# Optimization experiments

Hardware: AMD Instinct MI355X
Metric: run time of the kernel (lower is better)

The kernel has to match this reference:

```python
import jax, jax.numpy as jnp
import numpy as np

N_NODES = 50000
N_EDGES = 800000
IN_DIM = 128
HID = 128
HEADS = 4
OUT_DIM = 32
NEG_SLOPE = 0.2  # DGL GATConv default


def _gat_params(key, in_dim, out_feat, heads):
    k1, k2, k3 = jax.random.split(key, 3)
    s = 1.0 / np.sqrt(in_dim)
    W = jax.random.normal(k1, (in_dim, heads * out_feat), jnp.float32) * s
    attn_l = jax.random.normal(k2, (heads, out_feat), jnp.float32) * 0.1
    attn_r = jax.random.normal(k3, (heads, out_feat), jnp.float32) * 0.1
    b = jnp.zeros((heads * out_feat,), jnp.float32)
    return W, attn_l, attn_r, b


def setup_inputs() -> dict:
    key = jax.random.key(0)
    ks = jax.random.split(key, 10)
    inp = {
        "x_am": jax.random.normal(ks[0], (N_NODES, IN_DIM), jnp.float32),
        "x_ph": jax.random.normal(ks[1], (N_NODES, IN_DIM), jnp.float32),
        "exist": jax.random.uniform(ks[2], (N_EDGES,), jnp.float32),
        "am_exist": jax.random.uniform(ks[3], (N_EDGES,), jnp.float32),
        "src": jax.random.randint(ks[4], (N_EDGES,), 0, N_NODES, jnp.int32),
        "dst": jax.random.randint(ks[5], (N_EDGES,), 0, N_NODES, jnp.int32),
    }
    # layer 0 (input_dim -> hidden//head per head), layer 1 (hidden -> output_dim per head)
    inp["W0a"], inp["al0a"], inp["ar0a"], inp["b0a"] = _gat_params(ks[6], IN_DIM, HID // HEADS, HEADS)
    inp["W0p"], inp["al0p"], inp["ar0p"], inp["b0p"] = _gat_params(ks[7], IN_DIM, HID // HEADS, HEADS)
    inp["W1a"], inp["al1a"], inp["ar1a"], inp["b1a"] = _gat_params(ks[8], HID, OUT_DIM, HEADS)
    inp["W1p"], inp["al1p"], inp["ar1p"], inp["b1p"] = _gat_params(ks[9], HID, OUT_DIM, HEADS)
    return inp


def gat_conv(x, src, dst, W, attn_l, attn_r, b, edge_w, n_nodes):
    """DGL-style GATConv with edge_weight: out[i] = sum_{e: dst=i} softmax_i(LeakyReLU(el[src]+er[dst])) * w_e * ft[src]."""
    heads, outf = attn_l.shape
    ft = (x @ W).reshape(-1, heads, outf)                 # (N, H, F)
    el = jnp.sum(ft * attn_l, axis=-1)                    # (N, H)
    er = jnp.sum(ft * attn_r, axis=-1)                    # (N, H)
    e = jax.nn.leaky_relu(el[src] + er[dst], NEG_SLOPE)   # (E, H)
    emax = jax.ops.segment_max(e, dst, num_segments=n_nodes)
    emax = jnp.where(jnp.isfinite(emax), emax, 0.0)       # guard isolated nodes
    ex = jnp.exp(e - emax[dst])
    denom = jax.ops.segment_sum(ex, dst, num_segments=n_nodes)
    a = ex / jnp.maximum(denom[dst], 1e-9)                # edge softmax over incoming edges
    a = a * edge_w[:, None]                               # post-softmax edge weighting
    out = jax.ops.segment_sum(ft[src] * a[:, :, None], dst, num_segments=n_nodes)  # (N, H, F)
    return out + b.reshape(heads, outf)


def reference(x_am, x_ph, exist, am_exist,
              W0a, al0a, ar0a, b0a, W0p, al0p, ar0p, b0p,
              W1a, al1a, ar1a, b1a, W1p, al1p, ar1p, b1p,
              src, dst):
    n = x_am.shape[0]
    # layer 0: GATConv -> flatten -> ReLU (dropout rate 0 in eval)
    h_am = gat_conv(x_am, src, dst, W0a, al0a, ar0a, b0a, am_exist, n)
    h_ph = gat_conv(x_ph, src, dst, W0p, al0p, ar0p, b0p, exist, n)
    h_am = jax.nn.relu(h_am.reshape(n, -1))
    h_ph = jax.nn.relu(h_ph.reshape(n, -1))
    # layer 1 (last): GATConv -> mean over heads
    h_am = gat_conv(h_am, src, dst, W1a, al1a, ar1a, b1a, am_exist, n).mean(axis=1)
    h_ph = gat_conv(h_ph, src, dst, W1p, al1p, ar1p, b1p, exist, n).mean(axis=1)
    return (h_am, h_ph)
```

## Files before the change

kernel.cpp:

```cpp
#include <hip/hip_runtime.h>
#include <hip/hip_fp16.h>


typedef _Float16 f16x8 __attribute__((ext_vector_type(8)));
typedef float f32x4 __attribute__((ext_vector_type(4)));

struct GemmP { const void* X; const __half* Wt; const float *al, *ar; __half* Y; float *el, *er; };
struct ChP   { const __half* ft; const float *el, *er, *bias; void* out; };

__global__ void init_kernel(int* __restrict__ zero, int nzero,
                            const float* __restrict__ W0a, const float* __restrict__ W0p,
                            const float* __restrict__ W1a, const float* __restrict__ W1p,
                            __half* __restrict__ Wt) {
  int i = blockIdx.x * 256 + threadIdx.x;
  if (i < nzero) zero[i] = 0;
  {
    int m = i >> 14, idx = i & 16383;
    const float* W = (m == 0) ? W0a : (m == 1) ? W0p : (m == 2) ? W1a : W1p;
    int nn = idx >> 7, k = idx & 127;
    Wt[(size_t)m * 16384 + nn * 128 + k] = __float2half_rn(W[k * 128 + nn]);
  }
}

__global__ __launch_bounds__(256) void scan_kernel(const int* __restrict__ counts,
                                                   int* __restrict__ offsets,
                                                   int* __restrict__ sync,
                                                   int nb_stride, int n, int E) {
  __shared__ int lds[256];
  __shared__ int sbid, sprev;
  int* state = sync + 64;
  int* agg = state + nb_stride;
  int* incl = agg + nb_stride;
  int t = threadIdx.x;
  if (t == 0) sbid = atomicAdd(sync, 1);
  __syncthreads();
  int bid = sbid;
  int i = bid * 256 + t;
  int v = (i < n) ? counts[i] : 0;
  lds[t] = v;
  __syncthreads();
  for (int off = 1; off < 256; off <<= 1) {
    int x = (t >= off) ? lds[t - off] : 0;
    __syncthreads();
    lds[t] += x;
    __syncthreads();
  }
  int total = lds[255];
  if (t == 0) {
    if (bid == 0) {
      __hip_atomic_store(&incl[0], total, __ATOMIC_RELAXED, __HIP_MEMORY_SCOPE_AGENT);
      __hip_atomic_store(&state[0], 2, __ATOMIC_RELEASE, __HIP_MEMORY_SCOPE_AGENT);
      sprev = 0;
    } else {
      __hip_atomic_store(&agg[bid], total, __ATOMIC_RELAXED, __HIP_MEMORY_SCOPE_AGENT);
      __hip_atomic_store(&state[bid], 1, __ATOMIC_RELEASE, __HIP_MEMORY_SCOPE_AGENT);
    }
  }
  if (bid > 0 && t < 64) {
    int run = 0;
    int base = bid - 1;
    while (true) {
      int idx = base - t;
      int st = 2, val = 0;
      if (idx >= 0) {
        do {
          st = __hip_atomic_load(&state[idx], __ATOMIC_ACQUIRE, __HIP_MEMORY_SCOPE_AGENT);
        } while (st == 0);
        val = (st == 2)
                  ? __hip_atomic_load(&incl[idx], __ATOMIC_RELAXED, __HIP_MEMORY_SCOPE_AGENT)
                  : __hip_atomic_load(&agg[idx], __ATOMIC_RELAXED, __HIP_MEMORY_SCOPE_AGENT);
      }
      unsigned long long done = __ballot(st == 2);
      int firstDone = (int)__ffsll(done) - 1;
      int contrib = (firstDone < 0) ? val : ((t <= firstDone) ? val : 0);
#pragma unroll
      for (int o = 1; o < 64; o <<= 1) contrib += __shfl_xor(contrib, o);
      run += contrib;
      if (firstDone >= 0) break;
      base -= 64;
    }
    if (t == 0) {
      __hip_atomic_store(&incl[bid], run + total, __ATOMIC_RELAXED, __HIP_MEMORY_SCOPE_AGENT);
      __hip_atomic_store(&state[bid], 2, __ATOMIC_RELEASE, __HIP_MEMORY_SCOPE_AGENT);
      sprev = run;
    }
  }
  __syncthreads();
  int prev = sprev;
  if (i < n) offsets[i] = prev + lds[t] - v;
  if (i == 0) offsets[n] = E;
}

__global__ void fill_kernel(const int* __restrict__ src, const int* __restrict__ dst,
                            const float* __restrict__ exist, const float* __restrict__ am_exist,
                            const int* __restrict__ offs, const int* __restrict__ rank,
                            int4* __restrict__ edge16, int E) {
  int e = blockIdx.x * blockDim.x + threadIdx.x;
  if (e >= E) return;
  int d = dst[e];
  int pos = offs[d] + rank[e];
  edge16[pos] = make_int4(src[e], d, __float_as_int(am_exist[e]), __float_as_int(exist[e]));
}

template <int AFP16>
__device__ __forceinline__ void gemm_body(GemmP p, int bx, int n) {
  constexpr int LDH = 72;
  constexpr int LDE = 136;
  __shared__ __half lds[2 * 128 * LDH];
  __half* As = lds;
  __half* Ws = lds + 128 * LDH;
  int t = threadIdx.x;
  int row0 = bx << 7;
  int wv = t >> 6, lane = t & 63;
  int m = lane & 15, q = lane >> 4;

  f32x4 acc[2][8];
#pragma unroll
  for (int rt = 0; rt < 2; ++rt)
#pragma unroll
    for (int ct = 0; ct < 8; ++ct) acc[rt][ct] = (f32x4){0.f, 0.f, 0.f, 0.f};

#pragma unroll
  for (int kh = 0; kh < 2; ++kh) {
    __syncthreads();
    if (AFP16) {
      const __half* Xh = (const __half*)p.X;
#pragma unroll
      for (int i = 0; i < 4; ++i) {
        int c = t + (i << 8);
        int r = c >> 3, o8 = c & 7;
        uint4 v = make_uint4(0, 0, 0, 0);
        if (row0 + r < n)
          v = *(const uint4*)(Xh + (size_t)(row0 + r) * 128 + (kh << 6) + (o8 << 3));
        *(uint4*)(As + r * LDH + (o8 << 3)) = v;
      }
    } else {
      const float* Xf = (const float*)p.X;
#pragma unroll
      for (int i = 0; i < 8; ++i) {
        int c = t + (i << 8);
        int r = c >> 4, f4 = c & 15;
        float4 v = make_float4(0.f, 0.f, 0.f, 0.f);
        if (row0 + r < n)
          v = *(const float4*)(Xf + (size_t)(row0 + r) * 128 + (kh << 6) + (f4 << 2));
        union { __half h[4]; uint2 u; } pk;
        pk.h[0] = __float2half_rn(v.x); pk.h[1] = __float2half_rn(v.y);
        pk.h[2] = __float2half_rn(v.z); pk.h[3] = __float2half_rn(v.w);
        *(uint2*)(As + r * LDH + (f4 << 2)) = pk.u;
      }
    }
#pragma unroll
    for (int i = 0; i < 4; ++i) {
      int c = t + (i << 8);
      int r = c >> 3, o8 = c & 7;
      uint4 v = *(const uint4*)(p.Wt + (size_t)r * 128 + (kh << 6) + (o8 << 3));
      *(uint4*)(Ws + r * LDH + (o8 << 3)) = v;
    }
    __syncthreads();
#pragma unroll
    for (int kc = 0; kc < 2; ++kc) {
      f16x8 a0 = *(const f16x8*)(As + (wv * 32 + m) * LDH + kc * 32 + q * 8);
      f16x8 a1 = *(const f16x8*)(As + (wv * 32 + 16 + m) * LDH + kc * 32 + q * 8);
#pragma unroll
      for (int ct = 0; ct < 8; ++ct) {
        f16x8 b = *(const f16x8*)(Ws + (ct * 16 + m) * LDH + kc * 32 + q * 8);
        acc[0][ct] = __builtin_amdgcn_mfma_f32_16x16x32_f16(a0, b, acc[0][ct], 0, 0, 0);
        acc[1][ct] = __builtin_amdgcn_mfma_f32_16x16x32_f16(a1, b, acc[1][ct], 0, 0, 0);
      }
    }
  }
  __syncthreads();
#pragma unroll
  for (int rt = 0; rt < 2; ++rt) {
    int rbase = wv * 32 + rt * 16 + q * 4;
#pragma unroll
    for (int ct = 0; ct < 8; ++ct) {
      int col = ct * 16 + m;
#pragma unroll
      for (int r = 0; r < 4; ++r)
        lds[(rbase + r) * LDE + col] = __float2half_rn(acc[rt][ct][r]);
    }
  }
  __syncthreads();
  {
    int r = t & 127;
    int half = t >> 7;
    int row = row0 + r;
    if (row < n) {
      float e0 = 0.f, e1 = 0.f, r0 = 0.f, r1 = 0.f;
#pragma unroll
      for (int i = 0; i < 8; ++i) {
        int cbase = half * 64 + i * 8;
        f16x8 v = *(const f16x8*)(lds + r * LDE + cbase);
        *(uint4*)(p.Y + (size_t)row * 128 + cbase) = *(const uint4*)&v;
#pragma unroll
        for (int j = 0; j < 8; ++j) {
          float f = (float)v[j];
          float av = p.al[cbase + j];
          float rv = p.ar[cbase + j];
          if (((i * 8 + j) >> 5) == 0) { e0 = fmaf(f, av, e0); r0 = fmaf(f, rv, r0); }
          else                         { e1 = fmaf(f, av, e1); r1 = fmaf(f, rv, r1); }
        }
      }
      *(float2*)(p.el + (size_t)row * 4 + half * 2) = make_float2(e0, e1);
      *(float2*)(p.er + (size_t)row * 4 + half * 2) = make_float2(r0, r1);
    }
  }
}

template <int AFP16>
__global__ __launch_bounds__(256) void gemm_kernel(GemmP p0, GemmP p1, int n) {
  gemm_body<AFP16>(blockIdx.y ? p1 : p0, blockIdx.x, n);
}

__global__ __launch_bounds__(256) void hist_gemm0_kernel(
    GemmP p0, GemmP p1, int gg, int n,
    const int* __restrict__ dst, int* __restrict__ counts,
    int* __restrict__ rank, int E) {
  int b = blockIdx.x;
  if (b < 2 * gg) {
    gemm_body<0>((b >= gg) ? p1 : p0, (b >= gg) ? b - gg : b, n);
    return;
  }
  int e = (b - 2 * gg) * 256 + threadIdx.x;
  if (e < E) rank[e] = atomicAdd(&counts[dst[e]], 1);
}

template <int LAYER>
__global__ __launch_bounds__(256) void gather_kernel(ChP c0, ChP c1,
                                                     const int* __restrict__ offs,
                                                     const int4* __restrict__ edge16, int n) {
  int t = threadIdx.x;
  int w = t >> 6;
  int lane = t & 63;
  int node = blockIdx.x * 2 + (w >> 1);
  int ch = w & 1;
  if (node >= n) return;
  ChP P = ch ? c1 : c0;
  int hh = lane >> 4;
  int ce = lane & 7;

  int start = __builtin_amdgcn_readfirstlane(offs[node]);
  int end = __builtin_amdgcn_readfirstlane(offs[node + 1]);
  float er_h = P.er[(size_t)node * 4 + hh];
  const __half2* ftbase = (const __half2*)P.ft;
  const float* elb = P.el;
  const int* e32 = (const int*)edge16;

  float acc0 = 0.f, acc1 = 0.f, l = 0.f;
  int k = start;
  while (k + 8 <= end) {
    int4 ed[8];
#pragma unroll
    for (int j = 0; j < 8; ++j) ed[j] = edge16[k + j];
    int s_v = e32[(size_t)(k + ce) * 4];
    float el_v = elb[(size_t)s_v * 4 + hh];
    float ev = el_v + er_h;
    ev = (ev > 0.f) ? ev : 0.2f * ev;
    float x_v = __expf(ev);
#pragma unroll
    for (int j = 0; j < 8; ++j) {
      int s = ed[j].x;
      float wgt = __int_as_float(ch ? ed[j].w : ed[j].z);
      __half2 fh = ftbase[(size_t)s * 64 + lane];
      float x = __shfl(x_v, j, 16);
      l += x;
      float cv = x * wgt;
      acc0 = fmaf(cv, __low2float(fh), acc0);
      acc1 = fmaf(cv, __high2float(fh), acc1);
    }
    k += 8;
  }
  for (; k < end; ++k) {
    int4 ed = edge16[k];
    int s = ed.x;
    float wgt = __int_as_float(ch ? ed.w : ed.z);
    float el_s = elb[(size_t)s * 4 + hh];
    float ev = el_s + er_h;
    ev = (ev > 0.f) ? ev : 0.2f * ev;
    float x = __expf(ev);
    __half2 fh = ftbase[(size_t)s * 64 + lane];
    l += x;
    float cv = x * wgt;
    acc0 = fmaf(cv, __low2float(fh), acc0);
    acc1 = fmaf(cv, __high2float(fh), acc1);
  }

  float rl = 1.f / fmaxf(l, 1e-9f);
  float2 b2 = *(const float2*)(P.bias + lane * 2);
  float v0 = fmaf(acc0, rl, b2.x);
  float v1 = fmaf(acc1, rl, b2.y);
  if (LAYER == 0) {
    __half2 h = __floats2half2_rn(fmaxf(v0, 0.f), fmaxf(v1, 0.f));
    ((__half2*)P.out)[(size_t)node * 64 + lane] = h;
  } else {
    v0 += __shfl_xor(v0, 16); v1 += __shfl_xor(v1, 16);
    v0 += __shfl_xor(v0, 32); v1 += __shfl_xor(v1, 32);
    if (lane < 16) {
      *(float2*)((float*)P.out + (size_t)node * 32 + lane * 2) =
          make_float2(0.25f * v0, 0.25f * v1);
    }
  }
}

extern "C" void kernel_launch(void* const* d_in, const int* in_sizes, int n_in,
                              void* d_out, int out_size, void* d_ws, size_t ws_size,
                              hipStream_t stream) {
  const float* x_am = (const float*)d_in[0];
  const float* x_ph = (const float*)d_in[1];
  const float* exist = (const float*)d_in[2];
  const float* am_exist = (const float*)d_in[3];
  const int* src = (const int*)d_in[4];
  const int* dst = (const int*)d_in[5];
  const float* W0a = (const float*)d_in[6];
  const float* al0a = (const float*)d_in[7];
  const float* ar0a = (const float*)d_in[8];
  const float* b0a = (const float*)d_in[9];
  const float* W0p = (const float*)d_in[10];
  const float* al0p = (const float*)d_in[11];
  const float* ar0p = (const float*)d_in[12];
  const float* b0p = (const float*)d_in[13];
  const float* W1a = (const float*)d_in[14];
  const float* al1a = (const float*)d_in[15];
  const float* ar1a = (const float*)d_in[16];
  const float* b1a = (const float*)d_in[17];
  const float* W1p = (const float*)d_in[18];
  const float* al1p = (const float*)d_in[19];
  const float* ar1p = (const float*)d_in[20];
  const float* b1p = (const float*)d_in[21];

  int n = in_sizes[0] / 128;
  int E = in_sizes[2];
  int N_pad = (n + 255) & ~255;
  int nb = (n + 255) / 256;
  int NB_pad = (nb + 63) & ~63;

  size_t szN = (size_t)N_pad * 4;
  size_t szSync = (size_t)(64 + 3 * NB_pad) * 4;
  size_t szRank = (size_t)E * 4;
  size_t szOffs = (size_t)(N_pad + 8) * 4;
  size_t szE16 = (size_t)E * 16;
  size_t szFt16 = (size_t)n * 128 * 2;
  size_t szEl = (size_t)N_pad * 4 * 4;
  size_t szWt = (size_t)4 * 128 * 128 * 2;

  auto rnd = [](size_t b) { return (b + 255) & ~(size_t)255; };
  size_t fixed = rnd(szN) + rnd(szSync) + rnd(szRank) + rnd(szOffs) + rnd(szE16) +
                 4 * rnd(szEl) + rnd(szWt);
  bool dual = ws_size >= fixed + 4 * rnd(szFt16);

  char* p = (char*)d_ws;
  auto take = [&](size_t b) { char* q = p; p += (b + 255) & ~(size_t)255; return q; };
  int* counts = (int*)take(szN);
  int* sync = (int*)take(szSync);
  int* rank = (int*)take(szRank);
  int* offs = (int*)take(szOffs);
  int4* edge16 = (int4*)take(szE16);
  __half* Wt = (__half*)take(szWt);
  float* el_am = (float*)take(szEl);
  float* el_ph = (float*)take(szEl);
  float* er_am = (float*)take(szEl);
  float* er_ph = (float*)take(szEl);
  __half* ft_am = (__half*)take(szFt16);
  __half* ft_ph = dual ? (__half*)take(szFt16) : ft_am;
  __half* hb_am = (__half*)take(szFt16);
  __half* hb_ph = dual ? (__half*)take(szFt16) : hb_am;

  float* out_am = (float*)d_out;
  float* out_ph = out_am + (size_t)n * 32;

  int nzero = (int)((rnd(szN) + rnd(szSync)) / 4);
  int gg = (n + 127) / 128;
  int gw = (n + 1) / 2;
  int nhb = (E + 255) / 256;
  GemmP g0a{x_am, Wt,          al0a, ar0a, ft_am, el_am, er_am};
  GemmP g0p{x_ph, Wt + 16384,  al0p, ar0p, ft_ph, el_ph, er_ph};
  GemmP g1a{hb_am, Wt + 32768, al1a, ar1a, ft_am, el_am, er_am};
  GemmP g1p{hb_ph, Wt + 49152, al1p, ar1p, ft_ph, el_ph, er_ph};
  ChP c0a{ft_am, el_am, er_am, b0a, hb_am};
  ChP c0p{ft_ph, el_ph, er_ph, b0p, hb_ph};
  ChP c1a{ft_am, el_am, er_am, b1a, out_am};
  ChP c1p{ft_ph, el_ph, er_ph, b1p, out_ph};

  init_kernel<<<256, 256, 0, stream>>>(counts, nzero, W0a, W0p, W1a, W1p, Wt);

  if (dual) {
    hist_gemm0_kernel<<<2 * gg + nhb, 256, 0, stream>>>(g0a, g0p, gg, n,
                                                        dst, counts, rank, E);
    scan_kernel<<<nb, 256, 0, stream>>>(counts, offs, sync, NB_pad, n, E);
    fill_kernel<<<nhb, 256, 0, stream>>>(src, dst, exist, am_exist, offs, rank,
                                         edge16, E);
    gather_kernel<0><<<gw, 256, 0, stream>>>(c0a, c0p, offs, edge16, n);
    gemm_kernel<1><<<dim3(gg, 2), 256, 0, stream>>>(g1a, g1p, n);
    gather_kernel<1><<<gw, 256, 0, stream>>>(c1a, c1p, offs, edge16, n);
  } else {
    hist_gemm0_kernel<<<2 * gg + nhb, 256, 0, stream>>>(g0a, g0a, gg, n,
                                                        dst, counts, rank, E);
    scan_kernel<<<nb, 256, 0, stream>>>(counts, offs, sync, NB_pad, n, E);
    fill_kernel<<<nhb, 256, 0, stream>>>(src, dst, exist, am_exist, offs, rank,
                                         edge16, E);
    gather_kernel<0><<<gw, 256, 0, stream>>>(c0a, c0a, offs, edge16, n);
    gemm_kernel<1><<<dim3(gg, 2), 256, 0, stream>>>(g1a, g1a, n);
    gather_kernel<1><<<gw, 256, 0, stream>>>(c1a, c1a, offs, edge16, n);
    gemm_kernel<0><<<dim3(gg, 2), 256, 0, stream>>>(g0p, g0p, n);
    gather_kernel<0><<<gw, 256, 0, stream>>>(c0p, c0p, offs, edge16, n);
    gemm_kernel<1><<<dim3(gg, 2), 256, 0, stream>>>(g1p, g1p, n);
    gather_kernel<1><<<gw, 256, 0, stream>>>(c1p, c1p, offs, edge16, n);
  }
}
```

Before: 382.8 us.

## Stagger the two GAT channels so layer-1 GEMM overlaps the other channel's gather

Gathers now run one channel per kernel: four nodes per block, each wave taking one node, instead of both channels interleaved per block. The layer-1 GEMM of one channel is fused into the same launch as the gather of the other channel, so compute-bound GEMM blocks and memory-bound gather blocks share the GPU at the same time. Each gather kernel now touches only one channel's ft/el arrays, which may improve cache locality. The trade-off is an extra launch in the dual path and possible load imbalance between GEMM and gather blocks within the fused grid.

```diff
diff --git a/kernel.cpp b/kernel.cpp
--- a/kernel.cpp
+++ b/kernel.cpp
@@ -6,7 +6,7 @@
 typedef float f32x4 __attribute__((ext_vector_type(4)));
 
 struct GemmP { const void* X; const __half* Wt; const float *al, *ar; __half* Y; float *el, *er; };
-struct ChP   { const __half* ft; const float *el, *er, *bias; void* out; };
+struct ChP   { const __half* ft; const float *el, *er, *bias; void* out; int wsel; };
 
 __global__ void init_kernel(int* __restrict__ zero, int nzero,
                             const float* __restrict__ W0a, const float* __restrict__ W0p,
@@ -227,16 +227,10 @@
 }
 
 template <int LAYER>
-__global__ __launch_bounds__(256) void gather_kernel(ChP c0, ChP c1,
-                                                     const int* __restrict__ offs,
-                                                     const int4* __restrict__ edge16, int n) {
-  int t = threadIdx.x;
-  int w = t >> 6;
-  int lane = t & 63;
-  int node = blockIdx.x * 2 + (w >> 1);
-  int ch = w & 1;
+__device__ __forceinline__ void gather_body(ChP P, int node, int lane,
+                                            const int* __restrict__ offs,
+                                            const int4* __restrict__ edge16, int n) {
   if (node >= n) return;
-  ChP P = ch ? c1 : c0;
   int hh = lane >> 4;
   int ce = lane & 7;
 
@@ -246,6 +240,7 @@
   const __half2* ftbase = (const __half2*)P.ft;
   const float* elb = P.el;
   const int* e32 = (const int*)edge16;
+  int wsel = P.wsel;
 
   float acc0 = 0.f, acc1 = 0.f, l = 0.f;
   int k = start;
@@ -261,7 +256,7 @@
 #pragma unroll
     for (int j = 0; j < 8; ++j) {
       int s = ed[j].x;
-      float wgt = __int_as_float(ch ? ed[j].w : ed[j].z);
+      float wgt = __int_as_float(wsel ? ed[j].w : ed[j].z);
       __half2 fh = ftbase[(size_t)s * 64 + lane];
       float x = __shfl(x_v, j, 16);
       l += x;
@@ -274,7 +269,7 @@
   for (; k < end; ++k) {
     int4 ed = edge16[k];
     int s = ed.x;
-    float wgt = __int_as_float(ch ? ed.w : ed.z);
+    float wgt = __int_as_float(wsel ? ed.w : ed.z);
     float el_s = elb[(size_t)s * 4 + hh];
     float ev = el_s + er_h;
     ev = (ev > 0.f) ? ev : 0.2f * ev;
@@ -301,6 +296,28 @@
           make_float2(0.25f * v0, 0.25f * v1);
     }
   }
+}
+
+template <int LAYER>
+__global__ __launch_bounds__(256) void gather_sc_kernel(ChP cp, const int* __restrict__ offs,
+                                                        const int4* __restrict__ edge16, int n) {
+  int t = threadIdx.x;
+  int node = blockIdx.x * 4 + (t >> 6);
+  gather_body<LAYER>(cp, node, t & 63, offs, edge16, n);
+}
+
+template <int GLAYER>
+__global__ __launch_bounds__(256) void gemm_gather_kernel(
+    GemmP gp, ChP cp, int gg, int n,
+    const int* __restrict__ offs, const int4* __restrict__ edge16) {
+  int b = blockIdx.x;
+  if (b < gg) {
+    gemm_body<1>(gp, b, n);
+    return;
+  }
+  int t = threadIdx.x;
+  int node = (b - gg) * 4 + (t >> 6);
+  gather_body<GLAYER>(cp, node, t & 63, offs, edge16, n);
 }
 
 extern "C" void kernel_launch(void* const* d_in, const int* in_sizes, int n_in,
@@ -371,16 +388,16 @@
 
   int nzero = (int)((rnd(szN) + rnd(szSync)) / 4);
   int gg = (n + 127) / 128;
-  int gw = (n + 1) / 2;
+  int gsc = (n + 3) / 4;
   int nhb = (E + 255) / 256;
   GemmP g0a{x_am, Wt,          al0a, ar0a, ft_am, el_am, er_am};
   GemmP g0p{x_ph, Wt + 16384,  al0p, ar0p, ft_ph, el_ph, er_ph};
   GemmP g1a{hb_am, Wt + 32768, al1a, ar1a, ft_am, el_am, er_am};
   GemmP g1p{hb_ph, Wt + 49152, al1p, ar1p, ft_ph, el_ph, er_ph};
-  ChP c0a{ft_am, el_am, er_am, b0a, hb_am};
-  ChP c0p{ft_ph, el_ph, er_ph, b0p, hb_ph};
-  ChP c1a{ft_am, el_am, er_am, b1a, out_am};
-  ChP c1p{ft_ph, el_ph, er_ph, b1p, out_ph};
+  ChP c0a{ft_am, el_am, er_am, b0a, hb_am, 0};
+  ChP c0p{ft_ph, el_ph, er_ph, b0p, hb_ph, 1};
+  ChP c1a{ft_am, el_am, er_am, b1a, out_am, 0};
+  ChP c1p{ft_ph, el_ph, er_ph, b1p, out_ph, 1};
 
   init_kernel<<<256, 256, 0, stream>>>(counts, nzero, W0a, W0p, W1a, W1p, Wt);
 
@@ -390,21 +407,22 @@
     scan_kernel<<<nb, 256, 0, stream>>>(counts, offs, sync, NB_pad, n, E);
     fill_kernel<<<nhb, 256, 0, stream>>>(src, dst, exist, am_exist, offs, rank,
                                          edge16, E);
-    gather_kernel<0><<<gw, 256, 0, stream>>>(c0a, c0p, offs, edge16, n);
-    gemm_kernel<1><<<dim3(gg, 2), 256, 0, stream>>>(g1a, g1p, n);
-    gather_kernel<1><<<gw, 256, 0, stream>>>(c1a, c1p, offs, edge16, n);
+    gather_sc_kernel<0><<<gsc, 256, 0, stream>>>(c0a, offs, edge16, n);
+    gemm_gather_kernel<0><<<gg + gsc, 256, 0, stream>>>(g1a, c0p, gg, n, offs, edge16);
+    gemm_gather_kernel<1><<<gg + gsc, 256, 0, stream>>>(g1p, c1a, gg, n, offs, edge16);
+    gather_sc_kernel<1><<<gsc, 256, 0, stream>>>(c1p, offs, edge16, n);
   } else {
     hist_gemm0_kernel<<<2 * gg + nhb, 256, 0, stream>>>(g0a, g0a, gg, n,
                                                         dst, counts, rank, E);
     scan_kernel<<<nb, 256, 0, stream>>>(counts, offs, sync, NB_pad, n, E);
     fill_kernel<<<nhb, 256, 0, stream>>>(src, dst, exist, am_exist, offs, rank,
                                          edge16, E);
-    gather_kernel<0><<<gw, 256, 0, stream>>>(c0a, c0a, offs, edge16, n);
-    gemm_kernel<1><<<dim3(gg, 2), 256, 0, stream>>>(g1a, g1a, n);
-    gather_kernel<1><<<gw, 256, 0, stream>>>(c1a, c1a, offs, edge16, n);
-    gemm_kernel<0><<<dim3(gg, 2), 256, 0, stream>>>(g0p, g0p, n);
-    gather_kernel<0><<<gw, 256, 0, stream>>>(c0p, c0p, offs, edge16, n);
-    gemm_kernel<1><<<dim3(gg, 2), 256, 0, stream>>>(g1p, g1p, n);
-    gather_kernel<1><<<gw, 256, 0, stream>>>(c1p, c1p, offs, edge16, n);
-  }
-}
+    gather_sc_kernel<0><<<gsc, 256, 0, stream>>>(c0a, offs, edge16, n);
+    gemm_kernel<1><<<dim3(gg, 1), 256, 0, stream>>>(g1a, g1a, n);
+    gather_sc_kernel<1><<<gsc, 256, 0, stream>>>(c1a, offs, edge16, n);
+    gemm_kernel<0><<<dim3(gg, 1), 256, 0, stream>>>(g0p, g0p, n);
+    gather_sc_kernel<0><<<gsc, 256, 0, stream>>>(c0p, offs, edge16, n);
+    gemm_kernel<1><<<dim3(gg, 1), 256, 0, stream>>>(g1p, g1p, n);
+    gather_sc_kernel<1><<<gsc, 256, 0, stream>>>(c1p, offs, edge16, n);
+  }
+}
```

After: 524.5 us. +37.0%, slower.

## Halve GEMM row tile to 64 and read weight fragments directly from global

Applied to the files above, without the earlier changes.

Shrinks the per-block GEMM tile from 128 to 64 rows, doubling the number of blocks, and drops LDS staging of the weight matrix. Each wave now loads its B fragments straight from global or L2 memory. The el/er epilogue is reorganised to one head per thread. The intent is better occupancy and load spread with less LDS use and fewer LDS copies, at the cost of redundant global weight reads across waves and blocks.

```diff
diff --git a/kernel.cpp b/kernel.cpp
--- a/kernel.cpp
+++ b/kernel.cpp
@@ -106,19 +106,15 @@
 __device__ __forceinline__ void gemm_body(GemmP p, int bx, int n) {
   constexpr int LDH = 72;
   constexpr int LDE = 136;
-  __shared__ __half lds[2 * 128 * LDH];
-  __half* As = lds;
-  __half* Ws = lds + 128 * LDH;
+  __shared__ __half lds[64 * LDE];
   int t = threadIdx.x;
-  int row0 = bx << 7;
+  int row0 = bx << 6;
   int wv = t >> 6, lane = t & 63;
   int m = lane & 15, q = lane >> 4;
 
-  f32x4 acc[2][8];
-#pragma unroll
-  for (int rt = 0; rt < 2; ++rt)
-#pragma unroll
-    for (int ct = 0; ct < 8; ++ct) acc[rt][ct] = (f32x4){0.f, 0.f, 0.f, 0.f};
+  f32x4 acc[8];
+#pragma unroll
+  for (int ct = 0; ct < 8; ++ct) acc[ct] = (f32x4){0.f, 0.f, 0.f, 0.f};
 
 #pragma unroll
   for (int kh = 0; kh < 2; ++kh) {
@@ -126,18 +122,18 @@
     if (AFP16) {
       const __half* Xh = (const __half*)p.X;
 #pragma unroll
-      for (int i = 0; i < 4; ++i) {
+      for (int i = 0; i < 2; ++i) {
         int c = t + (i << 8);
         int r = c >> 3, o8 = c & 7;
         uint4 v = make_uint4(0, 0, 0, 0);
         if (row0 + r < n)
           v = *(const uint4*)(Xh + (size_t)(row0 + r) * 128 + (kh << 6) + (o8 << 3));
-        *(uint4*)(As + r * LDH + (o8 << 3)) = v;
+        *(uint4*)(lds + r * LDH + (o8 << 3)) = v;
       }
     } else {
       const float* Xf = (const float*)p.X;
 #pragma unroll
-      for (int i = 0; i < 8; ++i) {
+      for (int i = 0; i < 4; ++i) {
         int c = t + (i << 8);
         int r = c >> 4, f4 = c & 15;
         float4 v = make_float4(0.f, 0.f, 0.f, 0.f);
@@ -146,64 +142,51 @@
         union { __half h[4]; uint2 u; } pk;
         pk.h[0] = __float2half_rn(v.x); pk.h[1] = __float2half_rn(v.y);
         pk.h[2] = __float2half_rn(v.z); pk.h[3] = __float2half_rn(v.w);
-        *(uint2*)(As + r * LDH + (f4 << 2)) = pk.u;
-      }
-    }
-#pragma unroll
-    for (int i = 0; i < 4; ++i) {
-      int c = t + (i << 8);
-      int r = c >> 3, o8 = c & 7;
-      uint4 v = *(const uint4*)(p.Wt + (size_t)r * 128 + (kh << 6) + (o8 << 3));
-      *(uint4*)(Ws + r * LDH + (o8 << 3)) = v;
+        *(uint2*)(lds + r * LDH + (f4 << 2)) = pk.u;
+      }
     }
     __syncthreads();
 #pragma unroll
     for (int kc = 0; kc < 2; ++kc) {
-      f16x8 a0 = *(const f16x8*)(As + (wv * 32 + m) * LDH + kc * 32 + q * 8);
-      f16x8 a1 = *(const f16x8*)(As + (wv * 32 + 16 + m) * LDH + kc * 32 + q * 8);
+      f16x8 a0 = *(const f16x8*)(lds + (wv * 16 + m) * LDH + kc * 32 + q * 8);
 #pragma unroll
       for (int ct = 0; ct < 8; ++ct) {
-        f16x8 b = *(const f16x8*)(Ws + (ct * 16 + m) * LDH + kc * 32 + q * 8);
-        acc[0][ct] = __builtin_amdgcn_mfma_f32_16x16x32_f16(a0, b, acc[0][ct], 0, 0, 0);
-        acc[1][ct] = __builtin_amdgcn_mfma_f32_16x16x32_f16(a1, b, acc[1][ct], 0, 0, 0);
-      }
-    }
-  }
-  __syncthreads();
-#pragma unroll
-  for (int rt = 0; rt < 2; ++rt) {
-    int rbase = wv * 32 + rt * 16 + q * 4;
-#pragma unroll
-    for (int ct = 0; ct < 8; ++ct) {
-      int col = ct * 16 + m;
-#pragma unroll
-      for (int r = 0; r < 4; ++r)
-        lds[(rbase + r) * LDE + col] = __float2half_rn(acc[rt][ct][r]);
-    }
+        f16x8 b = *(const f16x8*)(p.Wt + (size_t)(ct * 16 + m) * 128 +
+                                  (kh << 6) + (kc << 5) + (q << 3));
+        acc[ct] = __builtin_amdgcn_mfma_f32_16x16x32_f16(a0, b, acc[ct], 0, 0, 0);
+      }
+    }
+  }
+  __syncthreads();
+#pragma unroll
+  for (int ct = 0; ct < 8; ++ct) {
+    int col = ct * 16 + m;
+    int rbase = wv * 16 + q * 4;
+#pragma unroll
+    for (int r = 0; r < 4; ++r)
+      lds[(rbase + r) * LDE + col] = __float2half_rn(acc[ct][r]);
   }
   __syncthreads();
   {
-    int r = t & 127;
-    int half = t >> 7;
+    int r = t & 63;
+    int q4 = t >> 6;
     int row = row0 + r;
     if (row < n) {
-      float e0 = 0.f, e1 = 0.f, r0 = 0.f, r1 = 0.f;
-#pragma unroll
-      for (int i = 0; i < 8; ++i) {
-        int cbase = half * 64 + i * 8;
+      float e0 = 0.f, r0 = 0.f;
+#pragma unroll
+      for (int i = 0; i < 4; ++i) {
+        int cbase = q4 * 32 + i * 8;
         f16x8 v = *(const f16x8*)(lds + r * LDE + cbase);
         *(uint4*)(p.Y + (size_t)row * 128 + cbase) = *(const uint4*)&v;
 #pragma unroll
         for (int j = 0; j < 8; ++j) {
           float f = (float)v[j];
-          float av = p.al[cbase + j];
-          float rv = p.ar[cbase + j];
-          if (((i * 8 + j) >> 5) == 0) { e0 = fmaf(f, av, e0); r0 = fmaf(f, rv, r0); }
-          else                         { e1 = fmaf(f, av, e1); r1 = fmaf(f, rv, r1); }
+          e0 = fmaf(f, p.al[cbase + j], e0);
+          r0 = fmaf(f, p.ar[cbase + j], r0);
         }
       }
-      *(float2*)(p.el + (size_t)row * 4 + half * 2) = make_float2(e0, e1);
-      *(float2*)(p.er + (size_t)row * 4 + half * 2) = make_float2(r0, r1);
+      p.el[(size_t)row * 4 + q4] = e0;
+      p.er[(size_t)row * 4 + q4] = r0;
     }
   }
 }
@@ -370,7 +353,7 @@
   float* out_ph = out_am + (size_t)n * 32;
 
   int nzero = (int)((rnd(szN) + rnd(szSync)) / 4);
-  int gg = (n + 127) / 128;
+  int gg = (n + 63) / 64;
   int gw = (n + 1) / 2;
   int nhb = (E + 255) / 256;
   GemmP g0a{x_am, Wt,          al0a, ar0a, ft_am, el_am, er_am};
```

Result: slower. 410.1 us (+7.1%).
